# Kernel tuning notes

Hardware: AMD Instinct MI355X
Metric: run time of the kernel (lower is better)

The kernel has to match this reference:

```python
import jax, jax.numpy as jnp
import numpy as np

N = 20000; E = 320000; F_IN = 128; H = 4; D = 32; HD = 128; G = 8; C = 10


def _ln(x, g, b):
    mu = x.mean(-1, keepdims=True)
    v = ((x - mu) ** 2).mean(-1, keepdims=True)
    return (x - mu) / jnp.sqrt(v + 1e-5) * g + b


def _tconv(x, src, dst, attr, Wq, Wk, Wv, We, Ws, bq, bk, bv, be, bs):
    # PyG TransformerConv (concat=True, beta=False, root_weight=True), eval mode
    n = x.shape[0]
    q = (x @ Wq + bq).reshape(n, H, D)[dst]            # [E,H,D] gather at targets i
    k = (x @ Wk + bk).reshape(n, H, D)[src]            # [E,H,D] gather at sources j
    v = (x @ Wv + bv).reshape(n, H, D)[src]
    ef = (attr @ We + be).reshape(-1, H, D)            # edge features lifted to [E,H,D]
    k = k + ef
    v = v + ef
    logit = (q * k).sum(-1) / jnp.sqrt(jnp.float32(D))  # [E,H]
    m = jax.ops.segment_max(logit, dst, num_segments=n)
    m = jnp.where(jnp.isfinite(m), m, 0.0)
    ex = jnp.exp(logit - m[dst])
    s = jax.ops.segment_sum(ex, dst, num_segments=n)
    alpha = ex / (s[dst] + 1e-16)                      # segment softmax over incoming edges
    out = jax.ops.segment_sum(v * alpha[..., None], dst, num_segments=n).reshape(n, HD)
    out = out + x @ Ws + bs                            # skip / root weight
    return out, alpha


def setup_inputs() -> dict:
    key = jax.random.key(0)
    ks = jax.random.split(key, 50)
    inp = {}
    inp["x"] = jax.random.normal(ks[0], (N, F_IN), jnp.float32)
    inp["edge_index"] = jax.random.randint(ks[1], (2, E), 0, N)
    inp["attr"] = jax.random.normal(ks[2], (E, 1), jnp.float32)
    inp["batch"] = jnp.sort(jax.random.randint(ks[3], (N,), 0, G))
    i = 4
    for l, din in zip((1, 2, 3), (F_IN, HD, HD)):
        for nm, shp in (("Wq", (din, HD)), ("Wk", (din, HD)), ("Wv", (din, HD)), ("We", (1, HD)), ("Ws", (din, HD))):
            inp[f"{nm}{l}"] = jax.random.normal(ks[i], shp, jnp.float32) * 0.05
            i += 1
        for nm in ("bq", "bk", "bv", "be", "bs"):
            inp[f"{nm}{l}"] = jnp.zeros((HD,), jnp.float32)
    inp["ln1_g"] = jnp.ones((HD,), jnp.float32); inp["ln1_b"] = jnp.zeros((HD,), jnp.float32)
    inp["ln2_g"] = jnp.ones((HD,), jnp.float32); inp["ln2_b"] = jnp.zeros((HD,), jnp.float32)
    inp["fc1_w"] = jax.random.normal(ks[i], (HD, HD), jnp.float32) * 0.05; i += 1
    inp["fc1_b"] = jnp.zeros((HD,), jnp.float32)
    inp["cln_g"] = jnp.ones((HD,), jnp.float32); inp["cln_b"] = jnp.zeros((HD,), jnp.float32)
    inp["fc2_w"] = jax.random.normal(ks[i], (HD, C), jnp.float32) * 0.05
    inp["fc2_b"] = jnp.zeros((C,), jnp.float32)
    return inp


def reference(x, edge_index, attr, batch,
              Wq1, Wk1, Wv1, We1, Ws1, bq1, bk1, bv1, be1, bs1,
              Wq2, Wk2, Wv2, We2, Ws2, bq2, bk2, bv2, be2, bs2,
              Wq3, Wk3, Wv3, We3, Ws3, bq3, bk3, bv3, be3, bs3,
              ln1_g, ln1_b, ln2_g, ln2_b,
              fc1_w, fc1_b, cln_g, cln_b, fc2_w, fc2_b):
    src, dst = edge_index[0], edge_index[1]
    h, a1 = _tconv(x, src, dst, attr, Wq1, Wk1, Wv1, We1, Ws1, bq1, bk1, bv1, be1, bs1)
    h = jax.nn.relu(_ln(h, ln1_g, ln1_b))              # dropout is identity in eval
    h, a2 = _tconv(h, src, dst, attr, Wq2, Wk2, Wv2, We2, Ws2, bq2, bk2, bv2, be2, bs2)
    h = jax.nn.relu(_ln(h, ln2_g, ln2_b))
    z, a3 = _tconv(h, src, dst, attr, Wq3, Wk3, Wv3, We3, Ws3, bq3, bk3, bv3, be3, bs3)
    # global mean pool over graphs
    cnt = jax.ops.segment_sum(jnp.ones((N,), z.dtype), batch, num_segments=G)
    z_pool = jax.ops.segment_sum(z, batch, num_segments=G) / jnp.maximum(cnt, 1.0)[:, None]
    # classifier
    hcl = jax.nn.relu(_ln(z_pool @ fc1_w + fc1_b, cln_g, cln_b))
    probs = jax.nn.softmax(hcl @ fc2_w + fc2_b, axis=1)
    z_sel = z_pool[batch[0]]
    return (z, z_sel, probs, a1, a2, a3)
```

## Files before the change

### kernel.cpp

```cpp
#include <hip/hip_runtime.h>


__device__ __forceinline__ unsigned pack_bf16_rne(float a, float b) {
    unsigned ua = __float_as_uint(a);
    ua += 0x7fffu + ((ua >> 16) & 1u);
    unsigned ub = __float_as_uint(b);
    ub += 0x7fffu + ((ub >> 16) & 1u);
    return (ua >> 16) | (ub & 0xffff0000u);
}

__global__ __launch_bounds__(256) void hist_kernel(const int* __restrict__ dst,
                                                   int* __restrict__ cnt, int E) {
    int e = blockIdx.x * 256 + threadIdx.x;
    if (e < E) atomicAdd(&cnt[dst[e]], 1);
}

__global__ __launch_bounds__(1024) void scan_kernel(const int* __restrict__ cnt,
                                                    int* __restrict__ rowptr, int n) {
    __shared__ int wls[16];
    __shared__ int carry;
    const int tid = threadIdx.x, lane = tid & 63, wid = tid >> 6;
    if (tid == 0) { carry = 0; rowptr[0] = 0; }
    __syncthreads();
    for (int base = 0; base < n; base += 1024) {
        int i = base + tid;
        int v = (i < n) ? cnt[i] : 0;
        int sc = v;
        for (int off = 1; off < 64; off <<= 1) {
            int t = __shfl_up(sc, off);
            if (lane >= off) sc += t;
        }
        if (lane == 63) wls[wid] = sc;
        __syncthreads();
        if (tid == 0) {
            int run = carry;
            for (int w2 = 0; w2 < 16; ++w2) { int t = wls[w2]; wls[w2] = run; run += t; }
            carry = run;
        }
        __syncthreads();
        if (i < n) rowptr[i + 1] = wls[wid] + sc;
        __syncthreads();
    }
}

__global__ __launch_bounds__(256) void fill_kernel(const int* __restrict__ src,
                                                   const int* __restrict__ dst,
                                                   const float* __restrict__ attr,
                                                   const int* __restrict__ rowptr,
                                                   int* __restrict__ tmp,
                                                   int* __restrict__ src_perm,
                                                   float* __restrict__ attr_perm,
                                                   int* __restrict__ eidp, int E) {
    int e = blockIdx.x * 256 + threadIdx.x;
    if (e < E) {
        int d = dst[e];
        int p = atomicAdd(&tmp[d], 1);
        int pos = rowptr[d] + p;
        src_perm[pos] = src[e];
        attr_perm[pos] = attr[e];
        eidp[pos] = e;
    }
}

__global__ __launch_bounds__(256) void gemm_qkvs_kernel(
    const float* __restrict__ X,
    const float* __restrict__ Wq, const float* __restrict__ Wk,
    const float* __restrict__ Wv, const float* __restrict__ Ws,
    const float* __restrict__ bq, const float* __restrict__ bk,
    const float* __restrict__ bv, const float* __restrict__ bs,
    float* __restrict__ qo, unsigned* __restrict__ ko,
    unsigned* __restrict__ vo, float* __restrict__ so, int nrows) {
    __shared__ float As[64][132];
    __shared__ float Bs[128][64];
    const int tid = threadIdx.x;
    const int row0 = blockIdx.x * 64;
    const int cb = blockIdx.y;
    const int w = cb >> 1;
    const int colbase = (cb & 1) * 64;
    const float* W    = (w == 0) ? Wq : (w == 1) ? Wk : (w == 2) ? Wv : Ws;
    const float* bias = (w == 0) ? bq : (w == 1) ? bk : (w == 2) ? bv : bs;

#pragma unroll
    for (int it = 0; it < 8; ++it) {
        int f = tid + it * 256;
        int r = f >> 5;
        int kq = f & 31;
        int row = row0 + r;
        float4 a = (row < nrows) ? *(const float4*)&X[(size_t)row * 128 + kq * 4]
                                 : make_float4(0.f, 0.f, 0.f, 0.f);
        *(float4*)&As[r][kq * 4] = a;
    }
#pragma unroll
    for (int it = 0; it < 8; ++it) {
        int f = tid + it * 256;
        int kk = f >> 4;
        int cq = f & 15;
        float4 b = *(const float4*)&W[(size_t)kk * 128 + colbase + cq * 4];
        *(float4*)&Bs[kk][cq * 4] = b;
    }
    __syncthreads();

    const int r0 = (tid >> 4) * 4;
    const int c0 = (tid & 15) * 4;
    float acc[4][4] = {};
#pragma unroll 8
    for (int kk = 0; kk < 128; ++kk) {
        const float4 b = *(const float4*)&Bs[kk][c0];
        const float a0 = As[r0 + 0][kk];
        const float a1 = As[r0 + 1][kk];
        const float a2 = As[r0 + 2][kk];
        const float a3 = As[r0 + 3][kk];
        acc[0][0] += a0 * b.x; acc[0][1] += a0 * b.y; acc[0][2] += a0 * b.z; acc[0][3] += a0 * b.w;
        acc[1][0] += a1 * b.x; acc[1][1] += a1 * b.y; acc[1][2] += a1 * b.z; acc[1][3] += a1 * b.w;
        acc[2][0] += a2 * b.x; acc[2][1] += a2 * b.y; acc[2][2] += a2 * b.z; acc[2][3] += a2 * b.w;
        acc[3][0] += a3 * b.x; acc[3][1] += a3 * b.y; acc[3][2] += a3 * b.z; acc[3][3] += a3 * b.w;
    }
    const float4 bb = *(const float4*)&bias[colbase + c0];
    if (w == 0 || w == 3) {
        float* OUT = (w == 0) ? qo : so;
#pragma unroll
        for (int i = 0; i < 4; ++i) {
            int row = row0 + r0 + i;
            if (row < nrows) {
                float4 o;
                o.x = acc[i][0] + bb.x; o.y = acc[i][1] + bb.y;
                o.z = acc[i][2] + bb.z; o.w = acc[i][3] + bb.w;
                *(float4*)&OUT[(size_t)row * 128 + colbase + c0] = o;
            }
        }
    } else {
        unsigned* OUT = (w == 1) ? ko : vo;
#pragma unroll
        for (int i = 0; i < 4; ++i) {
            int row = row0 + r0 + i;
            if (row < nrows) {
                unsigned u0 = pack_bf16_rne(acc[i][0] + bb.x, acc[i][1] + bb.y);
                unsigned u1 = pack_bf16_rne(acc[i][2] + bb.z, acc[i][3] + bb.w);
                *(uint2*)&OUT[(size_t)row * 64 + ((colbase + c0) >> 1)] = make_uint2(u0, u1);
            }
        }
    }
}

__global__ __launch_bounds__(256) void node_fused_kernel(
    const float* __restrict__ qb, const unsigned* __restrict__ kb,
    const unsigned* __restrict__ vb,
    const float* __restrict__ Wev, const float* __restrict__ bev,
    const int* __restrict__ rowptr, const int* __restrict__ src_perm,
    const float* __restrict__ attr_perm, const int* __restrict__ eidp,
    float* __restrict__ alpha_perm, float* __restrict__ alpha_out,
    float* __restrict__ out, int n) {
    __shared__ float alds[4][64][4];
    const int wid = threadIdx.x >> 6;
    const int node = blockIdx.x * 4 + wid;
    const int lane = threadIdx.x & 63;
    if (node >= n) return;
    const int start = rowptr[node], end = rowptr[node + 1];
    if (start == end) return;

    const float we0 = Wev[2 * lane], we1 = Wev[2 * lane + 1];
    const float be0 = bev[2 * lane], be1 = bev[2 * lane + 1];
    const float2 qv = *(const float2*)&qb[(size_t)node * 128 + 2 * lane];
    const float scale = 0.17677669529663687f;

    float mh = -1e30f;
    for (int c0 = start; c0 < end; c0 += 64) {
        const int nc = min(64, end - c0);
        const int sj = (lane < nc) ? src_perm[c0 + lane] : 0;
        const float aj = (lane < nc) ? attr_perm[c0 + lane] : 0.f;
        int t = 0;
        for (; t + 1 < nc; t += 2) {
            const int s0 = __shfl(sj, t), s1 = __shfl(sj, t + 1);
            const float a0 = __shfl(aj, t), a1 = __shfl(aj, t + 1);
            const unsigned u0 = kb[(size_t)s0 * 64 + lane];
            const unsigned u1 = kb[(size_t)s1 * 64 + lane];
            float p0 = qv.x * (__uint_as_float(u0 << 16) + a0 * we0 + be0)
                     + qv.y * (__uint_as_float(u0 & 0xffff0000u) + a0 * we1 + be1);
            float p1 = qv.x * (__uint_as_float(u1 << 16) + a1 * we0 + be0)
                     + qv.y * (__uint_as_float(u1 & 0xffff0000u) + a1 * we1 + be1);
#pragma unroll
            for (int off = 1; off < 16; off <<= 1) {
                p0 += __shfl_xor(p0, off);
                p1 += __shfl_xor(p1, off);
            }
            p0 *= scale; p1 *= scale;
            mh = fmaxf(mh, fmaxf(p0, p1));
            if ((lane & 15) == 0) {
                alpha_perm[(size_t)(c0 + t) * 4 + (lane >> 4)] = p0;
                alpha_perm[(size_t)(c0 + t + 1) * 4 + (lane >> 4)] = p1;
            }
        }
        if (t < nc) {
            const int s0 = __shfl(sj, t);
            const float a0 = __shfl(aj, t);
            const unsigned u0 = kb[(size_t)s0 * 64 + lane];
            float p0 = qv.x * (__uint_as_float(u0 << 16) + a0 * we0 + be0)
                     + qv.y * (__uint_as_float(u0 & 0xffff0000u) + a0 * we1 + be1);
#pragma unroll
            for (int off = 1; off < 16; off <<= 1) p0 += __shfl_xor(p0, off);
            p0 *= scale;
            mh = fmaxf(mh, p0);
            if ((lane & 15) == 0)
                alpha_perm[(size_t)(c0 + t) * 4 + (lane >> 4)] = p0;
        }
    }
    const float m0 = __shfl(mh, 0), m1 = __shfl(mh, 16);
    const float m2 = __shfl(mh, 32), m3 = __shfl(mh, 48);

    float4 s4 = make_float4(0.f, 0.f, 0.f, 0.f);
    for (int c0 = start; c0 < end; c0 += 64) {
        const int j = c0 + lane;
        if (j < end) {
            float4 lg = *(const float4*)&alpha_perm[(size_t)j * 4];
            lg.x = __expf(lg.x - m0); lg.y = __expf(lg.y - m1);
            lg.z = __expf(lg.z - m2); lg.w = __expf(lg.w - m3);
            *(float4*)&alpha_perm[(size_t)j * 4] = lg;
            s4.x += lg.x; s4.y += lg.y; s4.z += lg.z; s4.w += lg.w;
        }
    }
#pragma unroll
    for (int off = 1; off < 64; off <<= 1) {
        s4.x += __shfl_xor(s4.x, off); s4.y += __shfl_xor(s4.y, off);
        s4.z += __shfl_xor(s4.z, off); s4.w += __shfl_xor(s4.w, off);
    }
    const float i0 = 1.f / (s4.x + 1e-16f), i1 = 1.f / (s4.y + 1e-16f);
    const float i2 = 1.f / (s4.z + 1e-16f), i3 = 1.f / (s4.w + 1e-16f);
    const int h = lane >> 4;

    float acc0 = 0.f, acc1 = 0.f;
    for (int c0 = start; c0 < end; c0 += 64) {
        const int nc = min(64, end - c0);
        const int j = c0 + lane;
        if (lane < nc) {
            float4 ex = *(const float4*)&alpha_perm[(size_t)j * 4];
            float4 al;
            al.x = ex.x * i0; al.y = ex.y * i1; al.z = ex.z * i2; al.w = ex.w * i3;
            *(float4*)&alpha_out[(size_t)eidp[j] * 4] = al;
            *(float4*)&alds[wid][lane][0] = al;
        }
        const int sj = (lane < nc) ? src_perm[j] : 0;
        const float aj = (lane < nc) ? attr_perm[j] : 0.f;
        int t = 0;
        for (; t + 1 < nc; t += 2) {
            const int s0 = __shfl(sj, t), s1 = __shfl(sj, t + 1);
            const float a0 = __shfl(aj, t), a1 = __shfl(aj, t + 1);
            const float w0 = alds[wid][t][h];
            const float w1 = alds[wid][t + 1][h];
            const unsigned u0 = vb[(size_t)s0 * 64 + lane];
            const unsigned u1 = vb[(size_t)s1 * 64 + lane];
            acc0 += w0 * (__uint_as_float(u0 << 16) + a0 * we0 + be0)
                  + w1 * (__uint_as_float(u1 << 16) + a1 * we0 + be0);
            acc1 += w0 * (__uint_as_float(u0 & 0xffff0000u) + a0 * we1 + be1)
                  + w1 * (__uint_as_float(u1 & 0xffff0000u) + a1 * we1 + be1);
        }
        if (t < nc) {
            const int s0 = __shfl(sj, t);
            const float a0 = __shfl(aj, t);
            const float w0 = alds[wid][t][h];
            const unsigned u0 = vb[(size_t)s0 * 64 + lane];
            acc0 += w0 * (__uint_as_float(u0 << 16) + a0 * we0 + be0);
            acc1 += w0 * (__uint_as_float(u0 & 0xffff0000u) + a0 * we1 + be1);
        }
    }
    float2 o = *(float2*)&out[(size_t)node * 128 + 2 * lane];
    o.x += acc0; o.y += acc1;
    *(float2*)&out[(size_t)node * 128 + 2 * lane] = o;
}

__global__ __launch_bounds__(256) void ln_relu_kernel(float* __restrict__ h,
                                                      const float* __restrict__ g,
                                                      const float* __restrict__ b, int n) {
    const int row = (blockIdx.x * 256 + threadIdx.x) >> 6;
    const int lane = threadIdx.x & 63;
    if (row >= n) return;
    const float x0 = h[(size_t)row * 128 + lane];
    const float x1 = h[(size_t)row * 128 + 64 + lane];
    float s = x0 + x1;
    for (int off = 1; off < 64; off <<= 1) s += __shfl_xor(s, off);
    const float mu = s * (1.f / 128.f);
    const float d0 = x0 - mu, d1 = x1 - mu;
    float vs = d0 * d0 + d1 * d1;
    for (int off = 1; off < 64; off <<= 1) vs += __shfl_xor(vs, off);
    const float inv = rsqrtf(vs * (1.f / 128.f) + 1e-5f);
    h[(size_t)row * 128 + lane]      = fmaxf(d0 * inv * g[lane] + b[lane], 0.f);
    h[(size_t)row * 128 + 64 + lane] = fmaxf(d1 * inv * g[64 + lane] + b[64 + lane], 0.f);
}

__global__ __launch_bounds__(128) void pool_kernel(const float* __restrict__ z,
                                                   const int* __restrict__ batch,
                                                   float* __restrict__ pool,
                                                   int* __restrict__ gcnt, int n) {
    const int c = threadIdx.x;
    const int row0 = blockIdx.x * 32;
    if (row0 >= n) return;
    const int rend = min(row0 + 32, n);
    int cur = batch[row0];
    float acc = 0.f;
    int run = 0;
    for (int r = row0; r < rend; ++r) {
        const int g = batch[r];
        if (g != cur) {
            atomicAdd(&pool[cur * 128 + c], acc);
            if (c == 0) atomicAdd(&gcnt[cur], run);
            acc = 0.f; run = 0; cur = g;
        }
        acc += z[(size_t)r * 128 + c];
        ++run;
    }
    atomicAdd(&pool[cur * 128 + c], acc);
    if (c == 0) atomicAdd(&gcnt[cur], run);
}

__global__ __launch_bounds__(128) void classifier_kernel(
    const float* __restrict__ pool, const int* __restrict__ gcnt,
    const int* __restrict__ batch,
    const float* __restrict__ fc1_w, const float* __restrict__ fc1_b,
    const float* __restrict__ cg, const float* __restrict__ cbv,
    const float* __restrict__ fc2_w, const float* __restrict__ fc2_b,
    float* __restrict__ zsel, float* __restrict__ probs) {
    __shared__ float zp[8][128];
    __shared__ float hc[8][128];
    __shared__ float red[2];
    __shared__ float lgt[8][10];
    const int c = threadIdx.x;
    const int lane = c & 63, wid = c >> 6;
#pragma unroll
    for (int g = 0; g < 8; ++g)
        zp[g][c] = pool[g * 128 + c] / fmaxf((float)gcnt[g], 1.f);
    __syncthreads();
    zsel[c] = zp[batch[0]][c];

    float acc[8];
#pragma unroll
    for (int g = 0; g < 8; ++g) acc[g] = fc1_b[c];
    for (int k = 0; k < 128; ++k) {
        const float w = fc1_w[k * 128 + c];
#pragma unroll
        for (int g = 0; g < 8; ++g) acc[g] += zp[g][k] * w;
    }
#pragma unroll
    for (int g = 0; g < 8; ++g) {
        float s = acc[g];
        for (int off = 1; off < 64; off <<= 1) s += __shfl_xor(s, off);
        if (lane == 0) red[wid] = s;
        __syncthreads();
        const float mu = (red[0] + red[1]) * (1.f / 128.f);
        __syncthreads();
        const float d = acc[g] - mu;
        float s2 = d * d;
        for (int off = 1; off < 64; off <<= 1) s2 += __shfl_xor(s2, off);
        if (lane == 0) red[wid] = s2;
        __syncthreads();
        const float var = (red[0] + red[1]) * (1.f / 128.f);
        __syncthreads();
        hc[g][c] = fmaxf(d * rsqrtf(var + 1e-5f) * cg[c] + cbv[c], 0.f);
    }
    __syncthreads();
    if (c < 80) {
        const int g = c / 10, j = c - g * 10;
        float s = fc2_b[j];
        for (int k = 0; k < 128; ++k) s += hc[g][k] * fc2_w[k * 10 + j];
        lgt[g][j] = s;
    }
    __syncthreads();
    if (c < 8) {
        float mx = -1e30f;
#pragma unroll
        for (int j = 0; j < 10; ++j) mx = fmaxf(mx, lgt[c][j]);
        float ex[10];
        float sum = 0.f;
#pragma unroll
        for (int j = 0; j < 10; ++j) { ex[j] = expf(lgt[c][j] - mx); sum += ex[j]; }
#pragma unroll
        for (int j = 0; j < 10; ++j) probs[c * 10 + j] = ex[j] / sum;
    }
}


extern "C" void kernel_launch(void* const* d_in, const int* in_sizes, int n_in,
                              void* d_out, int out_size, void* d_ws, size_t ws_size,
                              hipStream_t stream) {
    const float* x = (const float*)d_in[0];
    const int* edge_index = (const int*)d_in[1];
    const float* attr = (const float*)d_in[2];
    const int* batch = (const int*)d_in[3];
    const int N = in_sizes[0] / 128;
    const int E = in_sizes[2];
    const int* src = edge_index;
    const int* dst = edge_index + E;

    const float *Wq[3], *Wk[3], *Wv[3], *We[3], *Ws[3];
    const float *bq[3], *bk[3], *bv[3], *be[3], *bs[3];
    int idx = 4;
    for (int l = 0; l < 3; ++l) {
        Wq[l] = (const float*)d_in[idx++];
        Wk[l] = (const float*)d_in[idx++];
        Wv[l] = (const float*)d_in[idx++];
        We[l] = (const float*)d_in[idx++];
        Ws[l] = (const float*)d_in[idx++];
        bq[l] = (const float*)d_in[idx++];
        bk[l] = (const float*)d_in[idx++];
        bv[l] = (const float*)d_in[idx++];
        be[l] = (const float*)d_in[idx++];
        bs[l] = (const float*)d_in[idx++];
    }
    const float* ln_g[2] = {(const float*)d_in[34], (const float*)d_in[36]};
    const float* ln_b[2] = {(const float*)d_in[35], (const float*)d_in[37]};
    const float* fc1_w = (const float*)d_in[38];
    const float* fc1_b = (const float*)d_in[39];
    const float* cln_g = (const float*)d_in[40];
    const float* cln_b = (const float*)d_in[41];
    const float* fc2_w = (const float*)d_in[42];
    const float* fc2_b = (const float*)d_in[43];
    const int C = in_sizes[43];

    float* out = (float*)d_out;
    float* z_out = out;
    float* zsel_out = out + (size_t)N * 128;
    float* probs_out = zsel_out + 128;
    const int GC = out_size - N * 128 - 128 - 3 * E * 4;
    const int G = GC / C;
    float* alpha_out[3];
    alpha_out[0] = probs_out + GC;
    alpha_out[1] = alpha_out[0] + (size_t)E * 4;
    alpha_out[2] = alpha_out[1] + (size_t)E * 4;

    char* p = (char*)d_ws;
    auto alloc = [&](size_t bytes) {
        void* r = (void*)p;
        p += (bytes + 255) & ~(size_t)255;
        return r;
    };
    float* qb = (float*)alloc((size_t)N * 128 * 4);
    unsigned* kb = (unsigned*)alloc((size_t)N * 64 * 4);
    unsigned* vb = (unsigned*)alloc((size_t)N * 64 * 4);
    float* hA = (float*)alloc((size_t)N * 128 * 4);
    float* hB = (float*)alloc((size_t)N * 128 * 4);
    int* counts = (int*)alloc((size_t)N * 4);
    int* rowptr = (int*)alloc((size_t)(N + 1) * 4);
    int* cnt2 = (int*)alloc((size_t)N * 4);
    int* src_perm = (int*)alloc((size_t)E * 4);
    float* attr_perm = (float*)alloc((size_t)E * 4);
    int* eidp = (int*)alloc((size_t)E * 4);
    float* alpha_perm = (float*)alloc((size_t)E * 4 * 4);
    float* pool = (float*)alloc((size_t)G * 128 * 4);
    int* gcnt = (int*)alloc((size_t)G * 4);

    hipMemsetAsync(counts, 0, (size_t)N * 4, stream);
    hipMemsetAsync(cnt2, 0, (size_t)N * 4, stream);
    hipMemsetAsync(pool, 0, (size_t)G * 128 * 4, stream);
    hipMemsetAsync(gcnt, 0, (size_t)G * 4, stream);

    hist_kernel<<<(E + 255) / 256, 256, 0, stream>>>(dst, counts, E);
    scan_kernel<<<1, 1024, 0, stream>>>(counts, rowptr, N);
    fill_kernel<<<(E + 255) / 256, 256, 0, stream>>>(src, dst, attr, rowptr, cnt2,
                                                     src_perm, attr_perm, eidp, E);

    const float* Xl = x;
    for (int l = 0; l < 3; ++l) {
        float* OUTl = (l == 0) ? hA : (l == 1) ? hB : z_out;
        gemm_qkvs_kernel<<<dim3((N + 63) / 64, 8), 256, 0, stream>>>(
            Xl, Wq[l], Wk[l], Wv[l], Ws[l], bq[l], bk[l], bv[l], bs[l],
            qb, kb, vb, OUTl, N);
        node_fused_kernel<<<(N + 3) / 4, 256, 0, stream>>>(
            qb, kb, vb, We[l], be[l], rowptr, src_perm, attr_perm, eidp,
            alpha_perm, alpha_out[l], OUTl, N);
        if (l < 2)
            ln_relu_kernel<<<((N + 3) / 4), 256, 0, stream>>>(OUTl, ln_g[l], ln_b[l], N);
        Xl = OUTl;
    }

    pool_kernel<<<(N + 31) / 32, 128, 0, stream>>>(z_out, batch, pool, gcnt, N);
    classifier_kernel<<<1, 128, 0, stream>>>(pool, gcnt, batch, fc1_w, fc1_b,
                                             cln_g, cln_b, fc2_w, fc2_b,
                                             zsel_out, probs_out);
}
```

Measured before the change: 552.1 us.

## Use bf16 MFMA GEMM, single-pass softmax for small degrees, bf16 LN output

Replaces the fp32 shared-memory GEMM with a bf16 MFMA kernel. Inputs and weights are prepacked to bf16: x by a convert kernel, weights by a transpose-pack kernel, and hidden states by ln_relu writing bf16 directly. Nodes with degree up to 64 now take a fast path that keeps logits and alphas in LDS, which avoids the global alpha_perm round trip and the extra passes. Together these cut GEMM compute time and edge-phase memory traffic. The cost is reduced input precision in the projections and a few extra small kernels.

Result: faster. 523.9 us (-5.1%).

```diff
diff --git a/kernel.cpp b/kernel.cpp
--- a/kernel.cpp
+++ b/kernel.cpp
@@ -1,5 +1,8 @@
 #include <hip/hip_runtime.h>
 
+
+typedef short short8v __attribute__((ext_vector_type(8)));
+typedef float f32x4 __attribute__((ext_vector_type(4)));
 
 __device__ __forceinline__ unsigned pack_bf16_rne(float a, float b) {
     unsigned ua = __float_as_uint(a);
@@ -7,6 +10,12 @@
     unsigned ub = __float_as_uint(b);
     ub += 0x7fffu + ((ub >> 16) & 1u);
     return (ua >> 16) | (ub & 0xffff0000u);
+}
+
+__device__ __forceinline__ unsigned short bf16_rne1(float a) {
+    unsigned u = __float_as_uint(a);
+    u += 0x7fffu + ((u >> 16) & 1u);
+    return (unsigned short)(u >> 16);
 }
 
 __global__ __launch_bounds__(256) void hist_kernel(const int* __restrict__ dst,
@@ -62,81 +71,78 @@
     }
 }
 
-__global__ __launch_bounds__(256) void gemm_qkvs_kernel(
-    const float* __restrict__ X,
-    const float* __restrict__ Wq, const float* __restrict__ Wk,
-    const float* __restrict__ Wv, const float* __restrict__ Ws,
+__global__ __launch_bounds__(256) void cvt_bf16_kernel(const float* __restrict__ in,
+                                                       unsigned* __restrict__ outp, int n32) {
+    int i = blockIdx.x * 256 + threadIdx.x;
+    if (i < n32) {
+        float2 v = *(const float2*)&in[(size_t)i * 2];
+        outp[i] = pack_bf16_rne(v.x, v.y);
+    }
+}
+
+__global__ __launch_bounds__(256) void prepack_kernel(
+    const float* __restrict__ W0, const float* __restrict__ W1,
+    const float* __restrict__ W2, const float* __restrict__ W3,
+    unsigned* __restrict__ wt) {
+    const int m = blockIdx.y;
+    const float* W = (m == 0) ? W0 : (m == 1) ? W1 : (m == 2) ? W2 : W3;
+    int idx = blockIdx.x * 256 + threadIdx.x;
+    int c = idx >> 6;
+    int kp = idx & 63;
+    float w0 = W[(size_t)(2 * kp) * 128 + c];
+    float w1 = W[(size_t)(2 * kp + 1) * 128 + c];
+    wt[(size_t)m * 8192 + (size_t)c * 64 + kp] = pack_bf16_rne(w0, w1);
+}
+
+__global__ __launch_bounds__(256) void gemm_mfma_kernel(
+    const unsigned short* __restrict__ Xb, const unsigned short* __restrict__ wt,
     const float* __restrict__ bq, const float* __restrict__ bk,
     const float* __restrict__ bv, const float* __restrict__ bs,
-    float* __restrict__ qo, unsigned* __restrict__ ko,
-    unsigned* __restrict__ vo, float* __restrict__ so, int nrows) {
-    __shared__ float As[64][132];
-    __shared__ float Bs[128][64];
-    const int tid = threadIdx.x;
-    const int row0 = blockIdx.x * 64;
-    const int cb = blockIdx.y;
-    const int w = cb >> 1;
-    const int colbase = (cb & 1) * 64;
-    const float* W    = (w == 0) ? Wq : (w == 1) ? Wk : (w == 2) ? Wv : Ws;
-    const float* bias = (w == 0) ? bq : (w == 1) ? bk : (w == 2) ? bv : bs;
-
-#pragma unroll
-    for (int it = 0; it < 8; ++it) {
-        int f = tid + it * 256;
-        int r = f >> 5;
-        int kq = f & 31;
-        int row = row0 + r;
-        float4 a = (row < nrows) ? *(const float4*)&X[(size_t)row * 128 + kq * 4]
-                                 : make_float4(0.f, 0.f, 0.f, 0.f);
-        *(float4*)&As[r][kq * 4] = a;
-    }
-#pragma unroll
-    for (int it = 0; it < 8; ++it) {
-        int f = tid + it * 256;
-        int kk = f >> 4;
-        int cq = f & 15;
-        float4 b = *(const float4*)&W[(size_t)kk * 128 + colbase + cq * 4];
-        *(float4*)&Bs[kk][cq * 4] = b;
-    }
-    __syncthreads();
-
-    const int r0 = (tid >> 4) * 4;
-    const int c0 = (tid & 15) * 4;
-    float acc[4][4] = {};
-#pragma unroll 8
-    for (int kk = 0; kk < 128; ++kk) {
-        const float4 b = *(const float4*)&Bs[kk][c0];
-        const float a0 = As[r0 + 0][kk];
-        const float a1 = As[r0 + 1][kk];
-        const float a2 = As[r0 + 2][kk];
-        const float a3 = As[r0 + 3][kk];
-        acc[0][0] += a0 * b.x; acc[0][1] += a0 * b.y; acc[0][2] += a0 * b.z; acc[0][3] += a0 * b.w;
-        acc[1][0] += a1 * b.x; acc[1][1] += a1 * b.y; acc[1][2] += a1 * b.z; acc[1][3] += a1 * b.w;
-        acc[2][0] += a2 * b.x; acc[2][1] += a2 * b.y; acc[2][2] += a2 * b.z; acc[2][3] += a2 * b.w;
-        acc[3][0] += a3 * b.x; acc[3][1] += a3 * b.y; acc[3][2] += a3 * b.z; acc[3][3] += a3 * b.w;
-    }
-    const float4 bb = *(const float4*)&bias[colbase + c0];
-    if (w == 0 || w == 3) {
-        float* OUT = (w == 0) ? qo : so;
-#pragma unroll
-        for (int i = 0; i < 4; ++i) {
-            int row = row0 + r0 + i;
-            if (row < nrows) {
-                float4 o;
-                o.x = acc[i][0] + bb.x; o.y = acc[i][1] + bb.y;
-                o.z = acc[i][2] + bb.z; o.w = acc[i][3] + bb.w;
-                *(float4*)&OUT[(size_t)row * 128 + colbase + c0] = o;
+    float* __restrict__ qo, unsigned short* __restrict__ ko,
+    unsigned short* __restrict__ vo, float* __restrict__ so, int nrows) {
+    const int lane = threadIdx.x & 63;
+    const int w = threadIdx.x >> 6;
+    const int m = blockIdx.y;
+    const int strip = blockIdx.x * 64 + w * 16;
+    const int arow = strip + (lane & 15);
+    const int arow_c = min(arow, nrows - 1);
+    const int kblk = (lane >> 4) * 8;
+    const unsigned short* Wm = wt + (size_t)m * 16384;
+    const float* bias = (m == 0) ? bq : (m == 1) ? bk : (m == 2) ? bv : bs;
+
+    f32x4 acc[8];
+#pragma unroll
+    for (int f = 0; f < 8; ++f) acc[f] = (f32x4){0.f, 0.f, 0.f, 0.f};
+
+#pragma unroll
+    for (int ks = 0; ks < 4; ++ks) {
+        const int k0 = ks * 32 + kblk;
+        const short8v a = *(const short8v*)&Xb[(size_t)arow_c * 128 + k0];
+#pragma unroll
+        for (int f = 0; f < 8; ++f) {
+            const short8v b = *(const short8v*)&Wm[(size_t)(f * 16 + (lane & 15)) * 128 + k0];
+            acc[f] = __builtin_amdgcn_mfma_f32_16x16x32_bf16(a, b, acc[f], 0, 0, 0);
+        }
+    }
+
+    const int r0 = strip + (lane >> 4) * 4;
+#pragma unroll
+    for (int f = 0; f < 8; ++f) {
+        const int col = f * 16 + (lane & 15);
+        const float bv_ = bias[col];
+        if (m == 0 || m == 3) {
+            float* OUT = (m == 0) ? qo : so;
+#pragma unroll
+            for (int r = 0; r < 4; ++r) {
+                int row = r0 + r;
+                if (row < nrows) OUT[(size_t)row * 128 + col] = acc[f][r] + bv_;
             }
-        }
-    } else {
-        unsigned* OUT = (w == 1) ? ko : vo;
-#pragma unroll
-        for (int i = 0; i < 4; ++i) {
-            int row = row0 + r0 + i;
-            if (row < nrows) {
-                unsigned u0 = pack_bf16_rne(acc[i][0] + bb.x, acc[i][1] + bb.y);
-                unsigned u1 = pack_bf16_rne(acc[i][2] + bb.z, acc[i][3] + bb.w);
-                *(uint2*)&OUT[(size_t)row * 64 + ((colbase + c0) >> 1)] = make_uint2(u0, u1);
+        } else {
+            unsigned short* OUT = (m == 1) ? ko : vo;
+#pragma unroll
+            for (int r = 0; r < 4; ++r) {
+                int row = r0 + r;
+                if (row < nrows) OUT[(size_t)row * 128 + col] = bf16_rne1(acc[f][r] + bv_);
             }
         }
     }
@@ -156,12 +162,104 @@
     const int lane = threadIdx.x & 63;
     if (node >= n) return;
     const int start = rowptr[node], end = rowptr[node + 1];
-    if (start == end) return;
+    const int deg = end - start;
+    if (deg == 0) return;
 
     const float we0 = Wev[2 * lane], we1 = Wev[2 * lane + 1];
     const float be0 = bev[2 * lane], be1 = bev[2 * lane + 1];
     const float2 qv = *(const float2*)&qb[(size_t)node * 128 + 2 * lane];
     const float scale = 0.17677669529663687f;
+    const int h = lane >> 4;
+
+    if (deg <= 64) {
+        const bool valid = lane < deg;
+        const int j = start + lane;
+        const int sj = valid ? src_perm[j] : 0;
+        const float aj = valid ? attr_perm[j] : 0.f;
+
+        int t = 0;
+        for (; t + 1 < deg; t += 2) {
+            const int s0 = __shfl(sj, t), s1 = __shfl(sj, t + 1);
+            const float a0 = __shfl(aj, t), a1 = __shfl(aj, t + 1);
+            const unsigned u0 = kb[(size_t)s0 * 64 + lane];
+            const unsigned u1 = kb[(size_t)s1 * 64 + lane];
+            float p0 = qv.x * (__uint_as_float(u0 << 16) + a0 * we0 + be0)
+                     + qv.y * (__uint_as_float(u0 & 0xffff0000u) + a0 * we1 + be1);
+            float p1 = qv.x * (__uint_as_float(u1 << 16) + a1 * we0 + be0)
+                     + qv.y * (__uint_as_float(u1 & 0xffff0000u) + a1 * we1 + be1);
+#pragma unroll
+            for (int off = 1; off < 16; off <<= 1) {
+                p0 += __shfl_xor(p0, off);
+                p1 += __shfl_xor(p1, off);
+            }
+            if ((lane & 15) == 0) {
+                alds[wid][t][h] = p0 * scale;
+                alds[wid][t + 1][h] = p1 * scale;
+            }
+        }
+        if (t < deg) {
+            const int s0 = __shfl(sj, t);
+            const float a0 = __shfl(aj, t);
+            const unsigned u0 = kb[(size_t)s0 * 64 + lane];
+            float p0 = qv.x * (__uint_as_float(u0 << 16) + a0 * we0 + be0)
+                     + qv.y * (__uint_as_float(u0 & 0xffff0000u) + a0 * we1 + be1);
+#pragma unroll
+            for (int off = 1; off < 16; off <<= 1) p0 += __shfl_xor(p0, off);
+            if ((lane & 15) == 0) alds[wid][t][h] = p0 * scale;
+        }
+
+        float4 lg = valid ? *(const float4*)&alds[wid][lane][0]
+                          : make_float4(-1e30f, -1e30f, -1e30f, -1e30f);
+        float4 mx = lg;
+#pragma unroll
+        for (int off = 1; off < 64; off <<= 1) {
+            mx.x = fmaxf(mx.x, __shfl_xor(mx.x, off));
+            mx.y = fmaxf(mx.y, __shfl_xor(mx.y, off));
+            mx.z = fmaxf(mx.z, __shfl_xor(mx.z, off));
+            mx.w = fmaxf(mx.w, __shfl_xor(mx.w, off));
+        }
+        float4 ev;
+        ev.x = __expf(lg.x - mx.x); ev.y = __expf(lg.y - mx.y);
+        ev.z = __expf(lg.z - mx.z); ev.w = __expf(lg.w - mx.w);
+        float4 s4 = ev;
+#pragma unroll
+        for (int off = 1; off < 64; off <<= 1) {
+            s4.x += __shfl_xor(s4.x, off); s4.y += __shfl_xor(s4.y, off);
+            s4.z += __shfl_xor(s4.z, off); s4.w += __shfl_xor(s4.w, off);
+        }
+        float4 al;
+        al.x = ev.x / (s4.x + 1e-16f); al.y = ev.y / (s4.y + 1e-16f);
+        al.z = ev.z / (s4.z + 1e-16f); al.w = ev.w / (s4.w + 1e-16f);
+        if (valid) *(float4*)&alpha_out[(size_t)eidp[j] * 4] = al;
+        *(float4*)&alds[wid][lane][0] = al;
+
+        float acc0 = 0.f, acc1 = 0.f;
+        t = 0;
+        for (; t + 1 < deg; t += 2) {
+            const int s0 = __shfl(sj, t), s1 = __shfl(sj, t + 1);
+            const float a0 = __shfl(aj, t), a1 = __shfl(aj, t + 1);
+            const float w0 = alds[wid][t][h];
+            const float w1 = alds[wid][t + 1][h];
+            const unsigned u0 = vb[(size_t)s0 * 64 + lane];
+            const unsigned u1 = vb[(size_t)s1 * 64 + lane];
+            acc0 += w0 * (__uint_as_float(u0 << 16) + a0 * we0 + be0)
+                  + w1 * (__uint_as_float(u1 << 16) + a1 * we0 + be0);
+            acc1 += w0 * (__uint_as_float(u0 & 0xffff0000u) + a0 * we1 + be1)
+                  + w1 * (__uint_as_float(u1 & 0xffff0000u) + a1 * we1 + be1);
+        }
+        if (t < deg) {
+            const int s0 = __shfl(sj, t);
+            const float a0 = __shfl(aj, t);
+            const float w0 = alds[wid][t][h];
+            const unsigned u0 = vb[(size_t)s0 * 64 + lane];
+            acc0 += w0 * (__uint_as_float(u0 << 16) + a0 * we0 + be0);
+            acc1 += w0 * (__uint_as_float(u0 & 0xffff0000u) + a0 * we1 + be1);
+        }
+        float2 o = *(float2*)&out[(size_t)node * 128 + 2 * lane];
+        o.x += acc0; o.y += acc1;
+        *(float2*)&out[(size_t)node * 128 + 2 * lane] = o;
+        return;
+    }
 
     float mh = -1e30f;
     for (int c0 = start; c0 < end; c0 += 64) {
@@ -186,8 +284,8 @@
             p0 *= scale; p1 *= scale;
             mh = fmaxf(mh, fmaxf(p0, p1));
             if ((lane & 15) == 0) {
-                alpha_perm[(size_t)(c0 + t) * 4 + (lane >> 4)] = p0;
-                alpha_perm[(size_t)(c0 + t + 1) * 4 + (lane >> 4)] = p1;
+                alpha_perm[(size_t)(c0 + t) * 4 + h] = p0;
+                alpha_perm[(size_t)(c0 + t + 1) * 4 + h] = p1;
             }
         }
         if (t < nc) {
@@ -200,8 +298,7 @@
             for (int off = 1; off < 16; off <<= 1) p0 += __shfl_xor(p0, off);
             p0 *= scale;
             mh = fmaxf(mh, p0);
-            if ((lane & 15) == 0)
-                alpha_perm[(size_t)(c0 + t) * 4 + (lane >> 4)] = p0;
+            if ((lane & 15) == 0) alpha_perm[(size_t)(c0 + t) * 4 + h] = p0;
         }
     }
     const float m0 = __shfl(mh, 0), m1 = __shfl(mh, 16);
@@ -225,7 +322,6 @@
     }
     const float i0 = 1.f / (s4.x + 1e-16f), i1 = 1.f / (s4.y + 1e-16f);
     const float i2 = 1.f / (s4.z + 1e-16f), i3 = 1.f / (s4.w + 1e-16f);
-    const int h = lane >> 4;
 
     float acc0 = 0.f, acc1 = 0.f;
     for (int c0 = start; c0 < end; c0 += 64) {
@@ -267,23 +363,28 @@
     *(float2*)&out[(size_t)node * 128 + 2 * lane] = o;
 }
 
-__global__ __launch_bounds__(256) void ln_relu_kernel(float* __restrict__ h,
+__global__ __launch_bounds__(256) void ln_relu_kernel(const float* __restrict__ hin,
+                                                      unsigned* __restrict__ hb,
                                                       const float* __restrict__ g,
                                                       const float* __restrict__ b, int n) {
     const int row = (blockIdx.x * 256 + threadIdx.x) >> 6;
     const int lane = threadIdx.x & 63;
     if (row >= n) return;
-    const float x0 = h[(size_t)row * 128 + lane];
-    const float x1 = h[(size_t)row * 128 + 64 + lane];
-    float s = x0 + x1;
+    const float2 xv = *(const float2*)&hin[(size_t)row * 128 + 2 * lane];
+    float s = xv.x + xv.y;
+#pragma unroll
     for (int off = 1; off < 64; off <<= 1) s += __shfl_xor(s, off);
     const float mu = s * (1.f / 128.f);
-    const float d0 = x0 - mu, d1 = x1 - mu;
+    const float d0 = xv.x - mu, d1 = xv.y - mu;
     float vs = d0 * d0 + d1 * d1;
+#pragma unroll
     for (int off = 1; off < 64; off <<= 1) vs += __shfl_xor(vs, off);
     const float inv = rsqrtf(vs * (1.f / 128.f) + 1e-5f);
-    h[(size_t)row * 128 + lane]      = fmaxf(d0 * inv * g[lane] + b[lane], 0.f);
-    h[(size_t)row * 128 + 64 + lane] = fmaxf(d1 * inv * g[64 + lane] + b[64 + lane], 0.f);
+    const float2 gv = *(const float2*)&g[2 * lane];
+    const float2 bv = *(const float2*)&b[2 * lane];
+    const float n0 = fmaxf(d0 * inv * gv.x + bv.x, 0.f);
+    const float n1 = fmaxf(d1 * inv * gv.y + bv.y, 0.f);
+    hb[(size_t)row * 64 + lane] = pack_bf16_rne(n0, n1);
 }
 
 __global__ __launch_bounds__(128) void pool_kernel(const float* __restrict__ z,
@@ -436,6 +537,9 @@
     unsigned* vb = (unsigned*)alloc((size_t)N * 64 * 4);
     float* hA = (float*)alloc((size_t)N * 128 * 4);
     float* hB = (float*)alloc((size_t)N * 128 * 4);
+    unsigned* xb = (unsigned*)alloc((size_t)N * 64 * 4);
+    unsigned* hb = (unsigned*)alloc((size_t)N * 64 * 4);
+    unsigned* wt = (unsigned*)alloc((size_t)12 * 8192 * 4);
     int* counts = (int*)alloc((size_t)N * 4);
     int* rowptr = (int*)alloc((size_t)(N + 1) * 4);
     int* cnt2 = (int*)alloc((size_t)N * 4);
@@ -456,18 +560,23 @@
     fill_kernel<<<(E + 255) / 256, 256, 0, stream>>>(src, dst, attr, rowptr, cnt2,
                                                      src_perm, attr_perm, eidp, E);
 
-    const float* Xl = x;
+    cvt_bf16_kernel<<<(N * 64 + 255) / 256, 256, 0, stream>>>(x, xb, N * 64);
+    for (int l = 0; l < 3; ++l)
+        prepack_kernel<<<dim3(32, 4), 256, 0, stream>>>(Wq[l], Wk[l], Wv[l], Ws[l],
+                                                        wt + (size_t)l * 4 * 8192);
+
     for (int l = 0; l < 3; ++l) {
         float* OUTl = (l == 0) ? hA : (l == 1) ? hB : z_out;
-        gemm_qkvs_kernel<<<dim3((N + 63) / 64, 8), 256, 0, stream>>>(
-            Xl, Wq[l], Wk[l], Wv[l], Ws[l], bq[l], bk[l], bv[l], bs[l],
-            qb, kb, vb, OUTl, N);
+        const unsigned short* Xin = (const unsigned short*)((l == 0) ? xb : hb);
+        gemm_mfma_kernel<<<dim3((N + 63) / 64, 4), 256, 0, stream>>>(
+            Xin, (const unsigned short*)(wt + (size_t)l * 4 * 8192),
+            bq[l], bk[l], bv[l], bs[l],
+            qb, (unsigned short*)kb, (unsigned short*)vb, OUTl, N);
         node_fused_kernel<<<(N + 3) / 4, 256, 0, stream>>>(
             qb, kb, vb, We[l], be[l], rowptr, src_perm, attr_perm, eidp,
             alpha_perm, alpha_out[l], OUTl, N);
         if (l < 2)
-            ln_relu_kernel<<<((N + 3) / 4), 256, 0, stream>>>(OUTl, ln_g[l], ln_b[l], N);
-        Xl = OUTl;
+            ln_relu_kernel<<<((N + 3) / 4), 256, 0, stream>>>(OUTl, hb, ln_g[l], ln_b[l], N);
     }
 
     pool_kernel<<<(N + 31) / 32, 128, 0, stream>>>(z_out, batch, pool, gcnt, N);
```
